# Performance work log

Measured on AMD Instinct MI355X. Metric: run time of the kernel, lower is better.

Reference implementation:

```python
import jax, jax.numpy as jnp
import numpy as np

B, N, D, U = 8, 2048, 512, 512

def setup_inputs() -> dict:
    key = jax.random.key(0)
    ks = jax.random.split(key, 7)
    s = 1.0 / np.sqrt(D)
    return {
        "inputs": jax.random.normal(ks[0], (B, N, D), dtype=jnp.float32),
        "Wq": jax.random.normal(ks[1], (D, U), dtype=jnp.float32) * s,
        "bq": jnp.zeros((U,), dtype=jnp.float32),
        "Wk": jax.random.normal(ks[2], (D, U), dtype=jnp.float32) * s,
        "bk": jnp.zeros((U,), dtype=jnp.float32),
        "Wv": jax.random.normal(ks[3], (D, U), dtype=jnp.float32) * s,
        "bv": jnp.zeros((U,), dtype=jnp.float32),
    }

def reference(inputs, Wq, bq, Wk, bk, Wv, bv):
    # Dense projections (Keras Dense: x @ W + b)
    Q = inputs @ Wq + bq  # [B, N, U]
    K = inputs @ Wk + bk  # [B, N, U]
    V = inputs @ Wv + bv  # [B, N, U]
    # NOTE: original module has NO 1/sqrt(d) scaling
    scores = jnp.einsum("bnu,bmu->bnm", Q, K)  # [B, N, N]
    attn = jax.nn.softmax(scores, axis=-1)
    return jnp.einsum("bnm,bmu->bnu", attn, V)  # [B, N, U]
```

## Files before the change

### kernel.cpp

```cpp
#include <hip/hip_runtime.h>


typedef _Float16 f16;
typedef _Float16 f16x4 __attribute__((ext_vector_type(4)));
typedef _Float16 f16x8 __attribute__((ext_vector_type(8)));
typedef float f32x4 __attribute__((ext_vector_type(4)));
typedef short s16x8 __attribute__((ext_vector_type(8)));
typedef unsigned short u16;

#define OFS 96.0f

__device__ __forceinline__ void stage16(const void* g, void* lds_uniform) {
    __builtin_amdgcn_global_load_lds(
        (const __attribute__((address_space(1))) void*)g,
        (__attribute__((address_space(3))) void*)lds_uniform,
        16, 0, 0);
}

__device__ __forceinline__ unsigned lds_off(const void* p) {
    return (unsigned)(size_t)(const __attribute__((address_space(3))) void*)p;
}

__device__ __forceinline__ f16x8 dsread16(unsigned a) {
    f16x8 r;
    asm volatile("ds_read_b128 %0, %1" : "=v"(r) : "v"(a));
    return r;
}

__device__ __forceinline__ u16 f2bf(float f) {
    unsigned u = __builtin_bit_cast(unsigned, f);
    u = (u + 0x7FFF + ((u >> 16) & 1)) >> 16;
    return (u16)u;
}
__device__ __forceinline__ float bf2f(u16 b) {
    return __builtin_bit_cast(float, (unsigned)b << 16);
}

__global__ __launch_bounds__(256) void prep_fused(
    const float* __restrict__ X,
    const float* __restrict__ Wq, const float* __restrict__ Wk,
    const float* __restrict__ Wv,
    const float* __restrict__ bq, const float* __restrict__ bk,
    const float* __restrict__ bv,
    f16* __restrict__ X16, f16* __restrict__ Wt, float* __restrict__ biases,
    float* __restrict__ rowsum) {
    __shared__ float t[32][33];
    const int bid = blockIdx.x, tid = threadIdx.x;
    if (bid < 8192) {
        int i = (bid * 256 + tid) * 4;
        float4 v = *(const float4*)(X + i);
        f16x4 o;
        o[0] = (f16)v.x; o[1] = (f16)v.y; o[2] = (f16)v.z; o[3] = (f16)v.w;
        *(f16x4*)(X16 + i) = o;
    } else if (bid < 8960) {
        int id = bid - 8192;
        int z = id >> 8, rem = id & 255;
        int u0 = (rem & 15) * 32, d0 = (rem >> 4) * 32;
        const float* W = (z == 0) ? Wq : (z == 1 ? Wk : Wv);
        f16* outp = Wt + (size_t)z * 262144;
        int tx = tid & 31, ty = tid >> 5;
#pragma unroll
        for (int r = 0; r < 4; r++)
            t[ty + 8 * r][tx] = W[(size_t)(d0 + ty + 8 * r) * 512 + u0 + tx];
        __syncthreads();
#pragma unroll
        for (int r = 0; r < 4; r++)
            outp[(size_t)(u0 + ty + 8 * r) * 512 + d0 + tx] = (f16)t[tx][ty + 8 * r];
    } else if (bid == 8960) {
#pragma unroll
        for (int j = 0; j < 6; j++) {
            int i = j * 256 + tid;
            float v = (i < 512) ? bq[i] : (i < 1024) ? bk[i - 512] : bv[i - 1024];
            biases[i] = v;
        }
    } else {
        int id = bid - 8961;
        float4 z4 = {0.f, 0.f, 0.f, 0.f};
        ((float4*)rowsum)[id * 256 + tid] = z4;
    }
}

template <int MODE>
__device__ __forceinline__ void gemm_core(
    const u16* __restrict__ A, int lda,
    const u16* __restrict__ Bt, int ldb,
    int m0, int n0, int K,
    const float* __restrict__ bias, float* __restrict__ rs,
    void* __restrict__ Cv, int ldc,
    u16* As, u16* Bs) {
    __shared__ float rowbuf[128];

    const int tid = threadIdx.x;
    const int wid = tid >> 6, lane = tid & 63;

    if (MODE == 2 || MODE == 4) {
        if (tid < 128) rowbuf[tid] = (MODE == 2 ? bias : rs)[m0 + tid];
    }

    const int schunk = (lane & 7) ^ ((lane >> 3) & 7);
    const u16* gA = A + (size_t)(m0 + wid * 32 + (lane >> 3)) * lda + schunk * 8;
    const u16* gB = Bt + (size_t)(n0 + wid * 32 + (lane >> 3)) * ldb + schunk * 8;
    u16* ldsA = As + (wid * 32) * 64;
    u16* ldsB = Bs + (wid * 32) * 64;

    const int wr = wid >> 1, wc = wid & 1;
    const int frow = lane & 15;
    const int f7 = frow & 7;
    const int c_lo = (lane >> 4) ^ f7;
    const int c_hi = ((lane >> 4) | 4) ^ f7;
    const u16* fA_lo = As + (wr * 64 + frow) * 64 + c_lo * 8;
    const u16* fA_hi = As + (wr * 64 + frow) * 64 + c_hi * 8;
    const u16* fB_lo = Bs + (wc * 64 + frow) * 64 + c_lo * 8;
    const u16* fB_hi = Bs + (wc * 64 + frow) * 64 + c_hi * 8;

    f32x4 acc[4][4] = {};

    for (int kt = 0; kt < K; kt += 64) {
#pragma unroll
        for (int j = 0; j < 4; j++)
            stage16(gA + (size_t)(j * 8) * lda, ldsA + (j * 8) * 64);
#pragma unroll
        for (int j = 0; j < 4; j++)
            stage16(gB + (size_t)(j * 8) * ldb, ldsB + (j * 8) * 64);
        gA += 64; gB += 64;
        __syncthreads();

#pragma unroll
        for (int half = 0; half < 2; half++) {
            const u16* pA = half ? fA_hi : fA_lo;
            const u16* pB = half ? fB_hi : fB_lo;
            if (MODE == 4) {
                s16x8 af[4], bf[4];
#pragma unroll
                for (int i = 0; i < 4; i++) af[i] = *(const s16x8*)(pA + i * 16 * 64);
#pragma unroll
                for (int i = 0; i < 4; i++) bf[i] = *(const s16x8*)(pB + i * 16 * 64);
#pragma unroll
                for (int mi = 0; mi < 4; mi++)
#pragma unroll
                    for (int ni = 0; ni < 4; ni++)
                        acc[mi][ni] = __builtin_amdgcn_mfma_f32_16x16x32_bf16(
                            af[mi], bf[ni], acc[mi][ni], 0, 0, 0);
            } else {
                f16x8 af[4], bf[4];
#pragma unroll
                for (int i = 0; i < 4; i++) af[i] = *(const f16x8*)(const f16*)(pA + i * 16 * 64);
#pragma unroll
                for (int i = 0; i < 4; i++) bf[i] = *(const f16x8*)(const f16*)(pB + i * 16 * 64);
#pragma unroll
                for (int mi = 0; mi < 4; mi++)
#pragma unroll
                    for (int ni = 0; ni < 4; ni++)
                        acc[mi][ni] = __builtin_amdgcn_mfma_f32_16x16x32_f16(
                            af[mi], bf[ni], acc[mi][ni], 0, 0, 0);
            }
        }
        __syncthreads();
    }

    const int crow0 = m0 + wr * 64 + ((lane >> 4) << 2);
    const int ccol0 = n0 + wc * 64 + (lane & 15);

    if (MODE == 1) {
        f16* C = (f16*)Cv;
#pragma unroll
        for (int mi = 0; mi < 4; mi++)
#pragma unroll
            for (int ni = 0; ni < 4; ni++) {
                float cb = bias[ccol0 + ni * 16];
#pragma unroll
                for (int r = 0; r < 4; r++)
                    C[(size_t)(crow0 + mi * 16 + r) * ldc + ccol0 + ni * 16] =
                        (f16)(acc[mi][ni][r] + cb);
            }
    } else if (MODE == 2) {
        u16* C = (u16*)Cv;
#pragma unroll
        for (int mi = 0; mi < 4; mi++)
#pragma unroll
            for (int ni = 0; ni < 4; ni++)
#pragma unroll
                for (int r = 0; r < 4; r++) {
                    float rb = rowbuf[crow0 + mi * 16 + r - m0];
                    C[(size_t)(crow0 + mi * 16 + r) * ldc + ccol0 + ni * 16] =
                        f2bf(acc[mi][ni][r] + rb);
                }
    } else {
        float* C = (float*)Cv;
#pragma unroll
        for (int mi = 0; mi < 4; mi++) {
            float inv[4];
#pragma unroll
            for (int r = 0; r < 4; r++)
                inv[r] = 1.0f / rowbuf[crow0 + mi * 16 + r - m0];
#pragma unroll
            for (int ni = 0; ni < 4; ni++)
#pragma unroll
                for (int r = 0; r < 4; r++)
                    C[(size_t)(crow0 + mi * 16 + r) * ldc + ccol0 + ni * 16] =
                        acc[mi][ni][r] * inv[r];
        }
    }
}

__global__ __launch_bounds__(256, 3) void proj_fused(
    const u16* __restrict__ X16, const u16* __restrict__ Wt,
    const float* __restrict__ biases,
    u16* __restrict__ QK, u16* __restrict__ Vt) {
    __shared__ __align__(16) u16 As[128 * 64];
    __shared__ __align__(16) u16 Bs[128 * 64];
    const int bid = blockIdx.x;
    if (bid < 1024) {
        int z = bid >> 9, rem = bid & 511;
        int bx = rem & 127, by = rem >> 7;
        gemm_core<1>(X16, 512, Wt + (size_t)z * 262144, 512,
                     bx * 128, by * 128, 512,
                     biases + z * 512, nullptr,
                     QK + (size_t)z * 8388608, 512, As, Bs);
    } else {
        int id = bid - 1024;
        int bz = id & 7, rem = id >> 3;
        int bx = rem & 3, by = rem >> 2;
        gemm_core<2>(Wt + (size_t)2 * 262144, 512,
                     X16 + (size_t)bz * 1048576, 512,
                     bx * 128, by * 128, 512,
                     biases + 1024, nullptr,
                     Vt + (size_t)bz * 1048576, 2048, As, Bs);
    }
}

__global__ __launch_bounds__(512, 2) void score_gemm(
    const u16* __restrict__ Q, const u16* __restrict__ Kk,
    u16* __restrict__ P, float* __restrict__ rowsum) {
    extern __shared__ __align__(16) char smem[];

    const int i = blockIdx.x;
    const int z = i & 7, y = (i >> 3) & 7, x = i >> 6;
    const int m0 = x * 256, n0 = y * 256;
    const u16* A  = Q  + (size_t)z * 1048576;
    const u16* Bt = Kk + (size_t)z * 1048576;
    u16* C = P + (size_t)z * 4194304;
    float* rs = rowsum + z * 2048;

    const int tid = threadIdx.x;
    const int wid = tid >> 6, lane = tid & 63;

    const int srow = lane >> 3;
    const int schunk = (lane & 7) ^ srow;
    const u16* gA0 = A  + (size_t)m0 * 512 + schunk * 8;
    const u16* gB0 = Bt + (size_t)n0 * 512 + schunk * 8;
    char* ldsbase = smem;

    auto stage_unit = [&](int u, int T, int b) {
        const u16* gm = (u < 2) ? gA0 : gB0;
        int rbase = (u & 1) * 128 + wid * 16;
        const u16* g = gm + (size_t)(rbase + srow) * 512 + T * 64;
        char* l = ldsbase + ((u < 2) ? 0 : 65536) + b * 32768 + rbase * 128;
        stage16(g, l);
        stage16(g + (size_t)8 * 512, l + 8 * 128);
    };

    const int wr = wid >> 2, wc = wid & 3;
    const int frow = lane & 15;
    const int f7 = frow & 7;
    const int c_lo = (lane >> 4) ^ f7;
    const int c_hi = ((lane >> 4) | 4) ^ f7;
    const unsigned smemB = lds_off(smem);
    const unsigned offA_lo = (unsigned)(((wr * 128 + frow) * 64 + c_lo * 8) * 2);
    const unsigned offA_hi = (unsigned)(((wr * 128 + frow) * 64 + c_hi * 8) * 2);
    const unsigned offB_lo = (unsigned)(((wc * 64 + frow) * 64 + c_lo * 8) * 2);
    const unsigned offB_hi = (unsigned)(((wc * 64 + frow) * 64 + c_hi * 8) * 2);

    f32x4 acc[8][4] = {};

    stage_unit(0, 0, 0); stage_unit(1, 0, 0);
    stage_unit(2, 0, 0); stage_unit(3, 0, 0);
    asm volatile("s_waitcnt vmcnt(0)" ::: "memory");
    asm volatile("s_barrier" ::: "memory");

#pragma unroll
    for (int T = 0; T < 8; ++T) {
        const int buf = T & 1;
        const unsigned baseA = smemB + (unsigned)(buf * 32768);
        const unsigned baseB = smemB + 65536u + (unsigned)(buf * 32768);

        f16x8 bf[4];
#pragma unroll
        for (int p = 0; p < 4; ++p) {
            const int kh = p >> 1, mh = p & 1;
            const unsigned aoff = baseA + (kh ? offA_hi : offA_lo);
            if (mh == 0) {
                const unsigned boff = baseB + (kh ? offB_hi : offB_lo);
#pragma unroll
                for (int ni = 0; ni < 4; ni++)
                    bf[ni] = dsread16(boff + (unsigned)(ni * 2048));
            }
            f16x8 af[4];
#pragma unroll
            for (int j = 0; j < 4; j++)
                af[j] = dsread16(aoff + (unsigned)((4 * mh + j) * 2048));

            if (T < 7) {
                if (p == 0) { stage_unit(0, T + 1, buf ^ 1); stage_unit(1, T + 1, buf ^ 1); }
                if (p == 1) { stage_unit(2, T + 1, buf ^ 1); stage_unit(3, T + 1, buf ^ 1); }
            }

            asm volatile("s_waitcnt lgkmcnt(0)" ::: "memory");
            __builtin_amdgcn_sched_barrier(0);
            __builtin_amdgcn_s_setprio(1);
#pragma unroll
            for (int j = 0; j < 4; j++)
#pragma unroll
                for (int ni = 0; ni < 4; ni++)
                    acc[4 * mh + j][ni] = __builtin_amdgcn_mfma_f32_16x16x32_f16(
                        af[j], bf[ni], acc[4 * mh + j][ni], 0, 0, 0);
            __builtin_amdgcn_s_setprio(0);

            if (p == 3)
                asm volatile("s_waitcnt vmcnt(0)" ::: "memory");
            asm volatile("s_barrier" ::: "memory");
        }
    }

    const int crow0 = m0 + wr * 128 + ((lane >> 4) << 2);
    const int ccol0 = n0 + wc * 64 + (lane & 15);
#pragma unroll
    for (int mi = 0; mi < 8; mi++)
#pragma unroll
        for (int r = 0; r < 4; r++) {
            float rsum = 0.0f;
#pragma unroll
            for (int ni = 0; ni < 4; ni++) {
                u16 b = f2bf(__expf(acc[mi][ni][r] - OFS));
                C[(size_t)(crow0 + mi * 16 + r) * 2048 + ccol0 + ni * 16] = b;
                rsum += bf2f(b);
            }
#pragma unroll
            for (int o = 1; o < 16; o <<= 1)
                rsum += __shfl_xor(rsum, o, 64);
            if ((lane & 15) == 0)
                atomicAdd(rs + crow0 + mi * 16 + r, rsum);
        }
}

__global__ __launch_bounds__(256) void pv_gemm(
    const u16* __restrict__ P, const u16* __restrict__ Vt,
    float* __restrict__ rowsum, float* __restrict__ out) {
    __shared__ __align__(16) u16 As[128 * 64];
    __shared__ __align__(16) u16 Bs[128 * 64];
    const int i = blockIdx.x;
    const int z = i & 7, y = (i >> 3) & 3, x = i >> 5;
    gemm_core<4>(P + (size_t)z * 4194304, 2048,
                 Vt + (size_t)z * 1048576, 2048,
                 x * 128, y * 128, 2048,
                 nullptr, rowsum + z * 2048,
                 out + (size_t)z * 1048576, 512, As, Bs);
}


extern "C" void kernel_launch(void* const* d_in, const int* in_sizes, int n_in,
                              void* d_out, int out_size, void* d_ws, size_t ws_size,
                              hipStream_t stream) {
    const float* X  = (const float*)d_in[0];
    const float* Wq = (const float*)d_in[1];
    const float* bq = (const float*)d_in[2];
    const float* Wk = (const float*)d_in[3];
    const float* bk = (const float*)d_in[4];
    const float* Wv = (const float*)d_in[5];
    const float* bv = (const float*)d_in[6];
    float* out = (float*)d_out;
    char* ws = (char*)d_ws;

    f16*   X16    = (f16*)ws;
    f16*   Wt     = (f16*)(ws + 16777216);
    float* biases = (float*)(ws + 18350080);
    u16*   QK     = (u16*)(ws + 18356224);
    u16*   Vt     = (u16*)(ws + 51910656);
    u16*   P      = (u16*)(ws + 68687872);
    float* rowsum = (float*)(ws + 135796736);

    static bool s_attr_done = false;
    if (!s_attr_done) {
        (void)hipFuncSetAttribute(reinterpret_cast<const void*>(score_gemm),
                                  hipFuncAttributeMaxDynamicSharedMemorySize,
                                  131072);
        s_attr_done = true;
    }

    prep_fused<<<8977, 256, 0, stream>>>(X, Wq, Wk, Wv, bq, bk, bv,
                                         X16, Wt, biases, rowsum);

    proj_fused<<<1536, 256, 0, stream>>>((const u16*)X16, (const u16*)Wt,
                                         biases, QK, Vt);

    score_gemm<<<512, 512, 131072, stream>>>(QK, QK + (size_t)8388608, P, rowsum);

    pv_gemm<<<512, 256, 0, stream>>>(P, Vt, rowsum, out);
}
```

Before: 208.8 us.

## Restructure score GEMM into 4-stage K=32 pipeline with prefetch distance two

Changes the score_gemm main loop from 8 double-buffered K=64 steps to 16 K=32 steps over a 4-slot LDS ring. The next-but-one tile is staged while the current one is consumed, with waits on vmcnt(4) so one tile's loads can stay in flight. A new packed row-pair swizzle keeps the LDS reads conflict-free. This gives fewer barriers per K unit of work and deeper overlap of global-to-LDS copies with MFMA, at the cost of more loop iterations and more delicate wait-count bookkeeping.

```diff
diff --git a/kernel.cpp b/kernel.cpp
--- a/kernel.cpp
+++ b/kernel.cpp
@@ -245,81 +245,93 @@
     const int tid = threadIdx.x;
     const int wid = tid >> 6, lane = tid & 63;
 
-    const int srow = lane >> 3;
-    const int schunk = (lane & 7) ^ srow;
-    const u16* gA0 = A  + (size_t)m0 * 512 + schunk * 8;
-    const u16* gB0 = Bt + (size_t)n0 * 512 + schunk * 8;
-    char* ldsbase = smem;
-
-    auto stage_unit = [&](int u, int T, int b) {
-        const u16* gm = (u < 2) ? gA0 : gB0;
-        int rbase = (u & 1) * 128 + wid * 16;
-        const u16* g = gm + (size_t)(rbase + srow) * 512 + T * 64;
-        char* l = ldsbase + ((u < 2) ? 0 : 65536) + b * 32768 + rbase * 128;
-        stage16(g, l);
-        stage16(g + (size_t)8 * 512, l + 8 * 128);
+    const int l3 = lane >> 3, l7 = lane & 7;
+    const int cA = l7 ^ l3;
+    const int rlocal = 2 * (l3) + (cA >> 2);
+    const int k16off = (cA & 3) * 8;
+
+    auto stageA = [&](int T) {
+        char* base = smem + (T & 3) * 16384 + (wid * 16) * 128;
+#pragma unroll
+        for (int j = 0; j < 2; j++) {
+            int row = m0 + 2 * (wid * 16 + j * 8) + rlocal;
+            const u16* g = A + (size_t)row * 512 + T * 32 + k16off;
+            stage16(g, base + j * 1024);
+        }
+    };
+    auto stageB = [&](int T) {
+        char* base = smem + 65536 + (T & 3) * 16384 + (wid * 16) * 128;
+#pragma unroll
+        for (int j = 0; j < 2; j++) {
+            int row = n0 + 2 * (wid * 16 + j * 8) + rlocal;
+            const u16* g = Bt + (size_t)row * 512 + T * 32 + k16off;
+            stage16(g, base + j * 1024);
+        }
     };
 
     const int wr = wid >> 2, wc = wid & 3;
     const int frow = lane & 15;
-    const int f7 = frow & 7;
-    const int c_lo = (lane >> 4) ^ f7;
-    const int c_hi = ((lane >> 4) | 4) ^ f7;
+    const int fs = frow >> 1;
+    const int fcc = (((frow & 1) << 2) | (lane >> 4)) ^ fs;
     const unsigned smemB = lds_off(smem);
-    const unsigned offA_lo = (unsigned)(((wr * 128 + frow) * 64 + c_lo * 8) * 2);
-    const unsigned offA_hi = (unsigned)(((wr * 128 + frow) * 64 + c_hi * 8) * 2);
-    const unsigned offB_lo = (unsigned)(((wc * 64 + frow) * 64 + c_lo * 8) * 2);
-    const unsigned offB_hi = (unsigned)(((wc * 64 + frow) * 64 + c_hi * 8) * 2);
+    const unsigned fA0 = (unsigned)((wr * 64) * 128 + fs * 128 + fcc * 16);
+    const unsigned fB0 = (unsigned)((wc * 32) * 128 + fs * 128 + fcc * 16);
 
     f32x4 acc[8][4] = {};
 
-    stage_unit(0, 0, 0); stage_unit(1, 0, 0);
-    stage_unit(2, 0, 0); stage_unit(3, 0, 0);
-    asm volatile("s_waitcnt vmcnt(0)" ::: "memory");
-    asm volatile("s_barrier" ::: "memory");
-
-#pragma unroll
-    for (int T = 0; T < 8; ++T) {
-        const int buf = T & 1;
-        const unsigned baseA = smemB + (unsigned)(buf * 32768);
-        const unsigned baseB = smemB + 65536u + (unsigned)(buf * 32768);
+    stageA(0); stageB(0);
+    stageA(1); stageB(1);
+    __builtin_amdgcn_sched_barrier(0);
+    asm volatile("s_waitcnt vmcnt(4)");
+    __builtin_amdgcn_s_barrier();
+
+#pragma unroll
+    for (int T = 0; T < 16; ++T) {
+        const unsigned aBase = smemB + (unsigned)((T & 3) * 16384);
+        const unsigned bBase = smemB + 65536u + (unsigned)((T & 3) * 16384);
 
         f16x8 bf[4];
 #pragma unroll
-        for (int p = 0; p < 4; ++p) {
-            const int kh = p >> 1, mh = p & 1;
-            const unsigned aoff = baseA + (kh ? offA_hi : offA_lo);
-            if (mh == 0) {
-                const unsigned boff = baseB + (kh ? offB_hi : offB_lo);
-#pragma unroll
-                for (int ni = 0; ni < 4; ni++)
-                    bf[ni] = dsread16(boff + (unsigned)(ni * 2048));
-            }
-            f16x8 af[4];
-#pragma unroll
-            for (int j = 0; j < 4; j++)
-                af[j] = dsread16(aoff + (unsigned)((4 * mh + j) * 2048));
-
-            if (T < 7) {
-                if (p == 0) { stage_unit(0, T + 1, buf ^ 1); stage_unit(1, T + 1, buf ^ 1); }
-                if (p == 1) { stage_unit(2, T + 1, buf ^ 1); stage_unit(3, T + 1, buf ^ 1); }
-            }
-
-            asm volatile("s_waitcnt lgkmcnt(0)" ::: "memory");
-            __builtin_amdgcn_sched_barrier(0);
-            __builtin_amdgcn_s_setprio(1);
-#pragma unroll
-            for (int j = 0; j < 4; j++)
-#pragma unroll
-                for (int ni = 0; ni < 4; ni++)
-                    acc[4 * mh + j][ni] = __builtin_amdgcn_mfma_f32_16x16x32_f16(
-                        af[j], bf[ni], acc[4 * mh + j][ni], 0, 0, 0);
-            __builtin_amdgcn_s_setprio(0);
-
-            if (p == 3)
-                asm volatile("s_waitcnt vmcnt(0)" ::: "memory");
-            asm volatile("s_barrier" ::: "memory");
-        }
+        for (int ni = 0; ni < 4; ni++)
+            bf[ni] = dsread16(bBase + fB0 + (unsigned)(ni * 1024));
+        f16x8 af[4];
+#pragma unroll
+        for (int j = 0; j < 4; j++)
+            af[j] = dsread16(aBase + fA0 + (unsigned)(j * 1024));
+        if (T < 14) stageA(T + 2);
+        __builtin_amdgcn_sched_barrier(0);
+        asm volatile("s_waitcnt lgkmcnt(0)");
+        __builtin_amdgcn_sched_barrier(0);
+        __builtin_amdgcn_s_setprio(1);
+#pragma unroll
+        for (int j = 0; j < 4; j++)
+#pragma unroll
+            for (int ni = 0; ni < 4; ni++)
+                acc[j][ni] = __builtin_amdgcn_mfma_f32_16x16x32_f16(
+                    af[j], bf[ni], acc[j][ni], 0, 0, 0);
+        __builtin_amdgcn_s_setprio(0);
+
+        f16x8 ag[4];
+#pragma unroll
+        for (int j = 0; j < 4; j++)
+            ag[j] = dsread16(aBase + fA0 + (unsigned)((4 + j) * 1024));
+        if (T < 14) stageB(T + 2);
+        __builtin_amdgcn_sched_barrier(0);
+        asm volatile("s_waitcnt lgkmcnt(0)");
+        __builtin_amdgcn_sched_barrier(0);
+        __builtin_amdgcn_s_setprio(1);
+#pragma unroll
+        for (int j = 0; j < 4; j++)
+#pragma unroll
+            for (int ni = 0; ni < 4; ni++)
+                acc[4 + j][ni] = __builtin_amdgcn_mfma_f32_16x16x32_f16(
+                    ag[j], bf[ni], acc[4 + j][ni], 0, 0, 0);
+        __builtin_amdgcn_s_setprio(0);
+
+        __builtin_amdgcn_sched_barrier(0);
+        if (T < 14)       asm volatile("s_waitcnt vmcnt(4)");
+        else if (T == 14) asm volatile("s_waitcnt vmcnt(0)");
+        if (T < 15) __builtin_amdgcn_s_barrier();
     }
 
     const int crow0 = m0 + wr * 128 + ((lane >> 4) << 2);
```

New measurement: 219.4 us. 1.05x slower.

## Fold Wq·Wkᵀ into one matrix and drop the K projection

Applied to the files above, without the earlier changes.

Reassociates the score computation as X·(Wq·Wkᵀ)·Xᵀ. A small new kernel forms the 512x512 product Wq·Wkᵀ in fp16, plus a per-row bias vector Wk·bq that keeps the column-dependent bias term. The projection stage then computes only G = X·M + rA and V, and the score GEMM uses the fp16 X directly as the key operand, removing the K projection GEMM and its 16 MB write. The new kernel is one extra launch, and its bias path is a single block doing serial, uncoalesced 512-element dot products, which could sit on the critical path. The bk terms are dropped on the grounds that softmax ignores row-constant shifts, and rounding the folded matrix to fp16 changes the numerics.

```diff
diff --git a/kernel.cpp b/kernel.cpp
--- a/kernel.cpp
+++ b/kernel.cpp
@@ -55,17 +55,27 @@
     } else if (bid < 8960) {
         int id = bid - 8192;
         int z = id >> 8, rem = id & 255;
-        int u0 = (rem & 15) * 32, d0 = (rem >> 4) * 32;
-        const float* W = (z == 0) ? Wq : (z == 1 ? Wk : Wv);
-        f16* outp = Wt + (size_t)z * 262144;
-        int tx = tid & 31, ty = tid >> 5;
-#pragma unroll
-        for (int r = 0; r < 4; r++)
-            t[ty + 8 * r][tx] = W[(size_t)(d0 + ty + 8 * r) * 512 + u0 + tx];
-        __syncthreads();
-#pragma unroll
-        for (int r = 0; r < 4; r++)
-            outp[(size_t)(u0 + ty + 8 * r) * 512 + d0 + tx] = (f16)t[tx][ty + 8 * r];
+        if (z < 2) {
+            const float* W = z ? Wk : Wq;
+            f16* outp = Wt + (size_t)z * 262144;
+            int i = rem * 1024 + tid * 4;
+            float4 v = *(const float4*)(W + i);
+            f16x4 o;
+            o[0] = (f16)v.x; o[1] = (f16)v.y; o[2] = (f16)v.z; o[3] = (f16)v.w;
+            *(f16x4*)(outp + i) = o;
+        } else {
+            int u0 = (rem & 15) * 32, d0 = (rem >> 4) * 32;
+            const float* W = Wv;
+            f16* outp = Wt + (size_t)2 * 262144;
+            int tx = tid & 31, ty = tid >> 5;
+#pragma unroll
+            for (int r = 0; r < 4; r++)
+                t[ty + 8 * r][tx] = W[(size_t)(d0 + ty + 8 * r) * 512 + u0 + tx];
+            __syncthreads();
+#pragma unroll
+            for (int r = 0; r < 4; r++)
+                outp[(size_t)(u0 + ty + 8 * r) * 512 + d0 + tx] = (f16)t[tx][ty + 8 * r];
+        }
     } else if (bid == 8960) {
 #pragma unroll
         for (int j = 0; j < 6; j++) {
@@ -173,6 +183,16 @@
                     C[(size_t)(crow0 + mi * 16 + r) * ldc + ccol0 + ni * 16] =
                         (f16)(acc[mi][ni][r] + cb);
             }
+    } else if (MODE == 5) {
+        f16* C = (f16*)Cv;
+#pragma unroll
+        for (int mi = 0; mi < 4; mi++)
+#pragma unroll
+            for (int ni = 0; ni < 4; ni++)
+#pragma unroll
+                for (int r = 0; r < 4; r++)
+                    C[(size_t)(crow0 + mi * 16 + r) * ldc + ccol0 + ni * 16] =
+                        (f16)acc[mi][ni][r];
     } else if (MODE == 2) {
         u16* C = (u16*)Cv;
 #pragma unroll
@@ -203,22 +223,45 @@
     }
 }
 
+__global__ __launch_bounds__(256) void wkq_gemm(
+    const u16* __restrict__ Wk16, const u16* __restrict__ Wq16,
+    const float* __restrict__ WkF, const float* __restrict__ bq,
+    u16* __restrict__ BtS, float* __restrict__ rA) {
+    __shared__ __align__(16) u16 As[128 * 64];
+    __shared__ __align__(16) u16 Bs[128 * 64];
+    const int b = blockIdx.x;
+    if (b < 16) {
+        int bx = b & 3, by = b >> 2;
+        gemm_core<5>(Wk16, 512, Wq16, 512, bx * 128, by * 128, 512,
+                     nullptr, nullptr, BtS, 512, As, Bs);
+    } else {
+        const int tid = threadIdx.x;
+#pragma unroll
+        for (int dd = 0; dd < 2; dd++) {
+            int d = tid + dd * 256;
+            const float* row = WkF + (size_t)d * 512;
+            float s = 0.0f;
+            for (int u = 0; u < 512; u++) s += row[u] * bq[u];
+            rA[d] = s;
+        }
+    }
+}
+
 __global__ __launch_bounds__(256, 3) void proj_fused(
     const u16* __restrict__ X16, const u16* __restrict__ Wt,
     const float* __restrict__ biases,
-    u16* __restrict__ QK, u16* __restrict__ Vt) {
+    const u16* __restrict__ BtS, const float* __restrict__ rA,
+    u16* __restrict__ G, u16* __restrict__ Vt) {
     __shared__ __align__(16) u16 As[128 * 64];
     __shared__ __align__(16) u16 Bs[128 * 64];
     const int bid = blockIdx.x;
-    if (bid < 1024) {
-        int z = bid >> 9, rem = bid & 511;
-        int bx = rem & 127, by = rem >> 7;
-        gemm_core<1>(X16, 512, Wt + (size_t)z * 262144, 512,
+    if (bid < 512) {
+        int bx = bid & 127, by = bid >> 7;
+        gemm_core<1>(X16, 512, BtS, 512,
                      bx * 128, by * 128, 512,
-                     biases + z * 512, nullptr,
-                     QK + (size_t)z * 8388608, 512, As, Bs);
+                     rA, nullptr, G, 512, As, Bs);
     } else {
-        int id = bid - 1024;
+        int id = bid - 512;
         int bz = id & 7, rem = id >> 3;
         int bx = rem & 3, by = rem >> 2;
         gemm_core<2>(Wt + (size_t)2 * 262144, 512,
@@ -374,7 +417,9 @@
     f16*   X16    = (f16*)ws;
     f16*   Wt     = (f16*)(ws + 16777216);
     float* biases = (float*)(ws + 18350080);
-    u16*   QK     = (u16*)(ws + 18356224);
+    u16*   G      = (u16*)(ws + 18356224);
+    u16*   BtS    = (u16*)(ws + 35133440);
+    float* rA     = (float*)(ws + 35657728);
     u16*   Vt     = (u16*)(ws + 51910656);
     u16*   P      = (u16*)(ws + 68687872);
     float* rowsum = (float*)(ws + 135796736);
@@ -390,10 +435,13 @@
     prep_fused<<<8977, 256, 0, stream>>>(X, Wq, Wk, Wv, bq, bk, bv,
                                          X16, Wt, biases, rowsum);
 
-    proj_fused<<<1536, 256, 0, stream>>>((const u16*)X16, (const u16*)Wt,
-                                         biases, QK, Vt);
-
-    score_gemm<<<512, 512, 131072, stream>>>(QK, QK + (size_t)8388608, P, rowsum);
+    wkq_gemm<<<17, 256, 0, stream>>>((const u16*)(Wt + 262144),
+                                     (const u16*)Wt, Wk, bq, BtS, rA);
+
+    proj_fused<<<1024, 256, 0, stream>>>((const u16*)X16, (const u16*)Wt,
+                                         biases, (const u16*)BtS, rA, G, Vt);
+
+    score_gemm<<<512, 512, 131072, stream>>>(G, (const u16*)X16, P, rowsum);
 
     pv_gemm<<<512, 256, 0, stream>>>(P, Vt, rowsum, out);
 }
```

Measured after the change: 232.4 us. +11.3%, slower.

## Widen PV GEMM tile to 128x256 with 512-thread blocks

Applied to the files above, without the earlier changes.

Replaces the generic 128x128 PV GEMM with a dedicated kernel that computes a 128x256 output tile per block using 8 waves, halving the block count. Each P tile loaded from global memory is now reused across twice as many V columns, which cuts P traffic, the dominant operand at 2048-long K. The cost is more LDS per block and fewer blocks (256) to spread across the CUs, which may reduce occupancy and leave load imbalance. The generic core loses its unused MODE 4 path.

```diff
diff --git a/kernel.cpp b/kernel.cpp
--- a/kernel.cpp
+++ b/kernel.cpp
@@ -93,8 +93,8 @@
     const int tid = threadIdx.x;
     const int wid = tid >> 6, lane = tid & 63;
 
-    if (MODE == 2 || MODE == 4) {
-        if (tid < 128) rowbuf[tid] = (MODE == 2 ? bias : rs)[m0 + tid];
+    if (MODE == 2) {
+        if (tid < 128) rowbuf[tid] = bias[m0 + tid];
     }
 
     const int schunk = (lane & 7) ^ ((lane >> 3) & 7);
@@ -129,31 +129,17 @@
         for (int half = 0; half < 2; half++) {
             const u16* pA = half ? fA_hi : fA_lo;
             const u16* pB = half ? fB_hi : fB_lo;
-            if (MODE == 4) {
-                s16x8 af[4], bf[4];
-#pragma unroll
-                for (int i = 0; i < 4; i++) af[i] = *(const s16x8*)(pA + i * 16 * 64);
-#pragma unroll
-                for (int i = 0; i < 4; i++) bf[i] = *(const s16x8*)(pB + i * 16 * 64);
-#pragma unroll
-                for (int mi = 0; mi < 4; mi++)
-#pragma unroll
-                    for (int ni = 0; ni < 4; ni++)
-                        acc[mi][ni] = __builtin_amdgcn_mfma_f32_16x16x32_bf16(
-                            af[mi], bf[ni], acc[mi][ni], 0, 0, 0);
-            } else {
-                f16x8 af[4], bf[4];
-#pragma unroll
-                for (int i = 0; i < 4; i++) af[i] = *(const f16x8*)(const f16*)(pA + i * 16 * 64);
-#pragma unroll
-                for (int i = 0; i < 4; i++) bf[i] = *(const f16x8*)(const f16*)(pB + i * 16 * 64);
-#pragma unroll
-                for (int mi = 0; mi < 4; mi++)
-#pragma unroll
-                    for (int ni = 0; ni < 4; ni++)
-                        acc[mi][ni] = __builtin_amdgcn_mfma_f32_16x16x32_f16(
-                            af[mi], bf[ni], acc[mi][ni], 0, 0, 0);
-            }
+            f16x8 af[4], bf[4];
+#pragma unroll
+            for (int i = 0; i < 4; i++) af[i] = *(const f16x8*)(const f16*)(pA + i * 16 * 64);
+#pragma unroll
+            for (int i = 0; i < 4; i++) bf[i] = *(const f16x8*)(const f16*)(pB + i * 16 * 64);
+#pragma unroll
+            for (int mi = 0; mi < 4; mi++)
+#pragma unroll
+                for (int ni = 0; ni < 4; ni++)
+                    acc[mi][ni] = __builtin_amdgcn_mfma_f32_16x16x32_f16(
+                        af[mi], bf[ni], acc[mi][ni], 0, 0, 0);
         }
         __syncthreads();
     }
@@ -173,7 +159,7 @@
                     C[(size_t)(crow0 + mi * 16 + r) * ldc + ccol0 + ni * 16] =
                         (f16)(acc[mi][ni][r] + cb);
             }
-    } else if (MODE == 2) {
+    } else {
         u16* C = (u16*)Cv;
 #pragma unroll
         for (int mi = 0; mi < 4; mi++)
@@ -185,21 +171,6 @@
                     C[(size_t)(crow0 + mi * 16 + r) * ldc + ccol0 + ni * 16] =
                         f2bf(acc[mi][ni][r] + rb);
                 }
-    } else {
-        float* C = (float*)Cv;
-#pragma unroll
-        for (int mi = 0; mi < 4; mi++) {
-            float inv[4];
-#pragma unroll
-            for (int r = 0; r < 4; r++)
-                inv[r] = 1.0f / rowbuf[crow0 + mi * 16 + r - m0];
-#pragma unroll
-            for (int ni = 0; ni < 4; ni++)
-#pragma unroll
-                for (int r = 0; r < 4; r++)
-                    C[(size_t)(crow0 + mi * 16 + r) * ldc + ccol0 + ni * 16] =
-                        acc[mi][ni][r] * inv[r];
-        }
     }
 }
 
@@ -343,18 +314,88 @@
         }
 }
 
-__global__ __launch_bounds__(256) void pv_gemm(
+__global__ __launch_bounds__(512) void pv_gemm(
     const u16* __restrict__ P, const u16* __restrict__ Vt,
     float* __restrict__ rowsum, float* __restrict__ out) {
     __shared__ __align__(16) u16 As[128 * 64];
-    __shared__ __align__(16) u16 Bs[128 * 64];
+    __shared__ __align__(16) u16 Bs[256 * 64];
+    __shared__ float rowbuf[128];
+
     const int i = blockIdx.x;
-    const int z = i & 7, y = (i >> 3) & 3, x = i >> 5;
-    gemm_core<4>(P + (size_t)z * 4194304, 2048,
-                 Vt + (size_t)z * 1048576, 2048,
-                 x * 128, y * 128, 2048,
-                 nullptr, rowsum + z * 2048,
-                 out + (size_t)z * 1048576, 512, As, Bs);
+    const int z = i & 7, y = (i >> 3) & 1, x = i >> 4;
+    const int m0 = x * 128, n0 = y * 256;
+    const u16* A  = P  + (size_t)z * 4194304;
+    const u16* Bt = Vt + (size_t)z * 1048576;
+    float* rs = rowsum + z * 2048;
+    float* C = out + (size_t)z * 1048576;
+
+    const int tid = threadIdx.x;
+    const int wid = tid >> 6, lane = tid & 63;
+
+    if (tid < 128) rowbuf[tid] = rs[m0 + tid];
+
+    const int schunk = (lane & 7) ^ ((lane >> 3) & 7);
+    const u16* gA = A + (size_t)(m0 + wid * 16 + (lane >> 3)) * 2048 + schunk * 8;
+    const u16* gB = Bt + (size_t)(n0 + wid * 32 + (lane >> 3)) * 2048 + schunk * 8;
+    u16* ldsA = As + (wid * 16) * 64;
+    u16* ldsB = Bs + (wid * 32) * 64;
+
+    const int wr = wid >> 2, wc = wid & 3;
+    const int frow = lane & 15;
+    const int f7 = frow & 7;
+    const int c_lo = (lane >> 4) ^ f7;
+    const int c_hi = ((lane >> 4) | 4) ^ f7;
+    const u16* fA_lo = As + (wr * 64 + frow) * 64 + c_lo * 8;
+    const u16* fA_hi = As + (wr * 64 + frow) * 64 + c_hi * 8;
+    const u16* fB_lo = Bs + (wc * 64 + frow) * 64 + c_lo * 8;
+    const u16* fB_hi = Bs + (wc * 64 + frow) * 64 + c_hi * 8;
+
+    f32x4 acc[4][4] = {};
+
+    for (int kt = 0; kt < 2048; kt += 64) {
+#pragma unroll
+        for (int j = 0; j < 2; j++)
+            stage16(gA + (size_t)(j * 8) * 2048, ldsA + (j * 8) * 64);
+#pragma unroll
+        for (int j = 0; j < 4; j++)
+            stage16(gB + (size_t)(j * 8) * 2048, ldsB + (j * 8) * 64);
+        gA += 64; gB += 64;
+        __syncthreads();
+
+#pragma unroll
+        for (int half = 0; half < 2; half++) {
+            const u16* pA = half ? fA_hi : fA_lo;
+            const u16* pB = half ? fB_hi : fB_lo;
+            s16x8 af[4], bf[4];
+#pragma unroll
+            for (int t = 0; t < 4; t++) af[t] = *(const s16x8*)(pA + t * 16 * 64);
+#pragma unroll
+            for (int t = 0; t < 4; t++) bf[t] = *(const s16x8*)(pB + t * 16 * 64);
+#pragma unroll
+            for (int mi = 0; mi < 4; mi++)
+#pragma unroll
+                for (int ni = 0; ni < 4; ni++)
+                    acc[mi][ni] = __builtin_amdgcn_mfma_f32_16x16x32_bf16(
+                        af[mi], bf[ni], acc[mi][ni], 0, 0, 0);
+        }
+        __syncthreads();
+    }
+
+    const int crow0 = m0 + wr * 64 + ((lane >> 4) << 2);
+    const int ccol0 = n0 + wc * 64 + (lane & 15);
+#pragma unroll
+    for (int mi = 0; mi < 4; mi++) {
+        float inv[4];
+#pragma unroll
+        for (int r = 0; r < 4; r++)
+            inv[r] = 1.0f / rowbuf[crow0 + mi * 16 + r - m0];
+#pragma unroll
+        for (int ni = 0; ni < 4; ni++)
+#pragma unroll
+            for (int r = 0; r < 4; r++)
+                C[(size_t)(crow0 + mi * 16 + r) * 512 + ccol0 + ni * 16] =
+                    acc[mi][ni][r] * inv[r];
+    }
 }
 
 
@@ -395,5 +436,5 @@
 
     score_gemm<<<512, 512, 131072, stream>>>(QK, QK + (size_t)8388608, P, rowsum);
 
-    pv_gemm<<<512, 256, 0, stream>>>(P, Vt, rowsum, out);
-}
+    pv_gemm<<<256, 512, 0, stream>>>(P, Vt, rowsum, out);
+}
```

Result: slower. 217.5 us (+4.2%).
